# Optimization experiments

Measured on AMD Instinct MI355X. Metric: run time of the kernel, lower is better.

## Reference

```python
import jax, jax.numpy as jnp
import numpy as np

B, T, D, H = 4, 2048, 1024, 16
HD = D // H
EPS = 1e-5


def gelu_tanh(x):
    c = jnp.sqrt(jnp.asarray(2.0 / jnp.pi, x.dtype))
    return 0.5 * x * (1.0 + jnp.tanh(c * (x + 0.044715 * x * x * x)))


def layernorm(x, gamma, beta):
    mean = jnp.mean(x, axis=-1, keepdims=True)
    var = jnp.var(x, axis=-1, keepdims=True)
    return gamma * (x - mean) / jnp.sqrt(var + EPS) + beta


def setup_inputs() -> dict:
    key = jax.random.key(0)
    ks = jax.random.split(key, 12)
    s = 0.02
    return {
        "x": jax.random.normal(ks[0], (B, T, D), jnp.float32),
        "Wq": jax.random.normal(ks[1], (D, D), jnp.float32) * s,
        "Wk": jax.random.normal(ks[2], (D, D), jnp.float32) * s,
        "Wv": jax.random.normal(ks[3], (D, D), jnp.float32) * s,
        "Wo": jax.random.normal(ks[4], (D, D), jnp.float32) * s,
        "bo": jnp.zeros((D,), jnp.float32),
        "W1": jax.random.normal(ks[5], (D, 4 * D), jnp.float32) * s,
        "b1": jnp.zeros((4 * D,), jnp.float32),
        "W2": jax.random.normal(ks[6], (4 * D, D), jnp.float32) * s,
        "b2": jnp.zeros((D,), jnp.float32),
        "gamma1": jnp.ones((D,), jnp.float32),
        "beta1": jnp.zeros((D,), jnp.float32),
        "gamma2": jnp.ones((D,), jnp.float32),
        "beta2": jnp.zeros((D,), jnp.float32),
    }


def reference(x, Wq, Wk, Wv, Wo, bo, W1, b1, W2, b2, gamma1, beta1, gamma2, beta2):
    # --- attention sublayer (pre-norm, causal) ---
    h = layernorm(x, gamma1, beta1)
    q = (h @ Wq).reshape(B, T, H, HD).transpose(0, 2, 1, 3)  # (B,H,T,hd)
    k = (h @ Wk).reshape(B, T, H, HD).transpose(0, 2, 1, 3)
    v = (h @ Wv).reshape(B, T, H, HD).transpose(0, 2, 1, 3)
    scores = jnp.einsum("bhqd,bhkd->bhqk", q, k) * (HD ** -0.5)
    causal = jnp.tril(jnp.ones((T, T), bool))
    scores = jnp.where(causal, scores, -jnp.inf)
    w = jax.nn.softmax(scores, axis=-1)
    attn = jnp.einsum("bhqk,bhkd->bhqd", w, v).transpose(0, 2, 1, 3).reshape(B, T, D)
    x = x + (attn @ Wo + bo)
    # --- FFN sublayer ---
    h2 = layernorm(x, gamma2, beta2)
    ff = gelu_tanh(h2 @ W1 + b1) @ W2 + b2
    return x + ff
```

## Files before the change

### kernel.cpp

```cpp
#include <hip/hip_runtime.h>
#include <hip/hip_bf16.h>


typedef __bf16 bf16;
typedef __attribute__((ext_vector_type(8))) __bf16 bf16x8;
typedef __attribute__((ext_vector_type(4))) __bf16 bf16x4;
typedef __attribute__((ext_vector_type(4))) float floatx4;

#define EXPC 0.18033688011112042f

__device__ __forceinline__ void async_cp16(const bf16* g, bf16* l) {
  __builtin_amdgcn_global_load_lds(
      (const __attribute__((address_space(1))) void*)g,
      (__attribute__((address_space(3))) void*)l, 16, 0, 0);
}

__global__ __launch_bounds__(256) void transpose_cvt4(
    const float* __restrict__ S0, const float* __restrict__ S1,
    const float* __restrict__ S2, const float* __restrict__ S3,
    bf16* __restrict__ D0, bf16* __restrict__ D1, bf16* __restrict__ D2,
    bf16* __restrict__ D3, int K, int N) {
  const float* W = (blockIdx.z == 0) ? S0 : (blockIdx.z == 1) ? S1
                   : (blockIdx.z == 2) ? S2 : S3;
  bf16* WT = (blockIdx.z == 0) ? D0 : (blockIdx.z == 1) ? D1
             : (blockIdx.z == 2) ? D2 : D3;
  __shared__ bf16 tile[32][33];
  const int tn = blockIdx.x;
  const int tk = blockIdx.y;
  const int t = threadIdx.x;
  const int row = t >> 3;
  const int c4 = (t & 7) * 4;

  const float* src = W + (size_t)(tk * 32 + row) * N + tn * 32 + c4;
  float4 v = *(const float4*)src;
  tile[row][c4 + 0] = (bf16)v.x;
  tile[row][c4 + 1] = (bf16)v.y;
  tile[row][c4 + 2] = (bf16)v.z;
  tile[row][c4 + 3] = (bf16)v.w;
  __syncthreads();
  bf16x4 o;
  o[0] = tile[c4 + 0][row];
  o[1] = tile[c4 + 1][row];
  o[2] = tile[c4 + 2][row];
  o[3] = tile[c4 + 3][row];
  *(bf16x4*)(WT + (size_t)(tn * 32 + row) * K + tk * 32 + c4) = o;
}

__global__ __launch_bounds__(256) void transpose_cvt(
    const float* __restrict__ W, bf16* __restrict__ WT, int K, int N) {
  __shared__ bf16 tile[32][33];
  const int tn = blockIdx.x;
  const int tk = blockIdx.y;
  const int t = threadIdx.x;
  const int row = t >> 3;
  const int c4 = (t & 7) * 4;

  const float* src = W + (size_t)(tk * 32 + row) * N + tn * 32 + c4;
  float4 v = *(const float4*)src;
  tile[row][c4 + 0] = (bf16)v.x;
  tile[row][c4 + 1] = (bf16)v.y;
  tile[row][c4 + 2] = (bf16)v.z;
  tile[row][c4 + 3] = (bf16)v.w;
  __syncthreads();
  bf16x4 o;
  o[0] = tile[c4 + 0][row];
  o[1] = tile[c4 + 1][row];
  o[2] = tile[c4 + 2][row];
  o[3] = tile[c4 + 3][row];
  *(bf16x4*)(WT + (size_t)(tn * 32 + row) * K + tk * 32 + c4) = o;
}

__global__ __launch_bounds__(256) void vtrans_kernel(
    const bf16* __restrict__ QKV, bf16* __restrict__ Vt) {
  const int tt = blockIdx.x;
  const int bh = blockIdx.y;
  const int b = bh >> 4, h = bh & 15;
  __shared__ bf16 tile[64][72];
  const int t = threadIdx.x;
  const int row = t >> 3;
  const int c8 = (t & 7) * 8;
  const size_t vbase = (size_t)b * 2048 * 3072 + 2048 + (size_t)h * 64;
  const bf16* src = QKV + vbase + (size_t)(tt * 64 + row) * 3072 + c8;
  *(bf16x8*)&tile[row][c8] = *(const bf16x8*)src;
  *(bf16x8*)&tile[row + 32][c8] = *(const bf16x8*)(src + (size_t)32 * 3072);
  __syncthreads();
  bf16x8 o0, o1;
#pragma unroll
  for (int j = 0; j < 8; ++j) {
    o0[j] = tile[c8 + j][row];
    o1[j] = tile[c8 + j][row + 32];
  }
  bf16* dst = Vt + ((size_t)bh * 64 + row) * 2048 + tt * 64 + c8;
  *(bf16x8*)dst = o0;
  *(bf16x8*)(dst + (size_t)32 * 2048) = o1;
}

__global__ __launch_bounds__(256) void ln_kernel(
    const float* __restrict__ x, const float* __restrict__ gamma,
    const float* __restrict__ beta, bf16* __restrict__ out) {
  const int row = blockIdx.x;
  const int t = threadIdx.x;
  const float* xr = x + (size_t)row * 1024;
  float4 v4 = *(const float4*)(xr + t * 4);
  float a[4] = {v4.x, v4.y, v4.z, v4.w};
  float s = a[0] + a[1] + a[2] + a[3];
  float ss = a[0] * a[0] + a[1] * a[1] + a[2] * a[2] + a[3] * a[3];
  for (int off = 1; off < 64; off <<= 1) {
    s += __shfl_xor(s, off);
    ss += __shfl_xor(ss, off);
  }
  __shared__ float red[8];
  const int wid = t >> 6, lane = t & 63;
  if (lane == 0) { red[wid] = s; red[wid + 4] = ss; }
  __syncthreads();
  s = red[0] + red[1] + red[2] + red[3];
  ss = red[4] + red[5] + red[6] + red[7];
  const float mean = s * (1.0f / 1024.0f);
  const float var = ss * (1.0f / 1024.0f) - mean * mean;
  const float rstd = rsqrtf(var + 1e-5f);
  bf16x4 o;
  for (int j = 0; j < 4; ++j) {
    float g = gamma[t * 4 + j];
    float b = beta[t * 4 + j];
    o[j] = (bf16)((a[j] - mean) * rstd * g + b);
  }
  *(bf16x4*)(out + (size_t)row * 1024 + t * 4) = o;
}

__device__ __forceinline__ float gelu_f(float x) {
  const float c = 0.7978845608028654f;
  float u = c * (x + 0.044715f * x * x * x);
  u = fminf(fmaxf(u, -10.0f), 10.0f);
  float t = __builtin_exp2f(u * 2.8853900817779268f);
  return x * t * __builtin_amdgcn_rcpf(t + 1.0f);
}

template <int MODE, int BK>
__global__ __launch_bounds__(256, 2) void gemm_bt(
    const bf16* __restrict__ A, const bf16* __restrict__ BT,
    const float* __restrict__ bias, const float* __restrict__ resid,
    void* __restrict__ out, int M, int N, int K) {
  __shared__ bf16 sA[128 * BK];
  __shared__ bf16 sB[128 * BK];
  constexpr int GPR = BK / 8;
  constexpr int CPT = GPR / 2;
  constexpr int RPI = 256 / GPR;
  constexpr int SW = (BK >= 64) ? 7 : 0;

  const int t = threadIdx.x;
  const int lane = t & 63, wid = t >> 6;
  const int waveM = wid >> 1, waveN = wid & 1;
  const int quad = lane >> 4, l16 = lane & 15;
  const size_t m0 = (size_t)blockIdx.x * 128;
  const size_t n0 = (size_t)blockIdx.y * 128;

  floatx4 acc[4][4] = {};

  const int r0 = t / GPR;
  const int gp = t % GPR;
  const int gsrc = gp ^ (r0 & SW);
  const bf16* Ag = A + (m0 + r0) * (size_t)K + gsrc * 8;
  const bf16* Bg = BT + (n0 + r0) * (size_t)K + gsrc * 8;
  bf16* sAp = sA + t * 8;
  bf16* sBp = sB + t * 8;

  for (int k0 = 0; k0 < K; k0 += BK) {
    __syncthreads();
#pragma unroll
    for (int it = 0; it < CPT; ++it) {
      async_cp16(Ag + k0 + (size_t)(it * RPI) * K, sAp + it * 2048);
      async_cp16(Bg + k0 + (size_t)(it * RPI) * K, sBp + it * 2048);
    }
    __syncthreads();
#pragma unroll
    for (int ks = 0; ks < BK / 32; ++ks) {
      bf16x8 af[4], bfv[4];
#pragma unroll
      for (int i = 0; i < 4; ++i) {
        const int rowA = waveM * 64 + i * 16 + l16;
        const int g = ((ks * 4 + quad) ^ (l16 & SW)) * 8;
        af[i] = *(const bf16x8*)&sA[rowA * BK + g];
        const int rowB = waveN * 64 + i * 16 + l16;
        bfv[i] = *(const bf16x8*)&sB[rowB * BK + g];
      }
#pragma unroll
      for (int mt = 0; mt < 4; ++mt)
#pragma unroll
        for (int nt = 0; nt < 4; ++nt)
          acc[mt][nt] = __builtin_amdgcn_mfma_f32_16x16x32_bf16(
              af[mt], bfv[nt], acc[mt][nt], 0, 0, 0);
    }
  }

#pragma unroll
  for (int mt = 0; mt < 4; ++mt) {
#pragma unroll
    for (int nt = 0; nt < 4; ++nt) {
      const size_t row_base = m0 + waveM * 64 + mt * 16 + quad * 4;
      const size_t col = n0 + waveN * 64 + nt * 16 + l16;
#pragma unroll
      for (int r = 0; r < 4; ++r) {
        const size_t row = row_base + r;
        float v = acc[mt][nt][r];
        if (MODE == 1) {
          v = gelu_f(v + bias[col]);
          ((bf16*)out)[row * N + col] = (bf16)v;
        } else if (MODE == 2) {
          v += bias[col] + resid[row * N + col];
          ((float*)out)[row * N + col] = v;
        } else {
          ((bf16*)out)[row * N + col] = (bf16)v;
        }
      }
    }
  }
}

__global__ __launch_bounds__(256) void attn_kernel(
    const bf16* __restrict__ QKV, const bf16* __restrict__ Vt,
    bf16* __restrict__ O) {
  const int idx = blockIdx.x;
  const int qt = 15 - (idx >> 6);
  const int bh = idx & 63;
  const int b = bh >> 4, h = bh & 15;
  const int t = threadIdx.x;
  const int lane = t & 63, wid = t >> 6;
  const int quad = lane >> 4, l16 = lane & 15;

  __shared__ bf16 sQ[128 * 64];
  __shared__ bf16 sK[64 * 64];
  __shared__ bf16 sV[64 * 64];
  __shared__ bf16 sP[4][16][72];

  const size_t qkvbase = (size_t)b * 2048 * 3072 + (size_t)h * 64;
  const int q0 = qt * 128;

  const int r0 = t >> 3;
  const int gp = t & 7;
  const int gsw = gp ^ (r0 & 7);

  {
    const bf16* pQ = QKV + qkvbase + (size_t)(q0 + r0) * 3072 + gsw * 8;
#pragma unroll
    for (int j = 0; j < 4; ++j)
      async_cp16(pQ + (size_t)(j * 32) * 3072, sQ + j * 2048 + t * 8);
  }

  const bf16* pK = QKV + qkvbase + 1024 + (size_t)r0 * 3072 + gsw * 8;
  const bf16* pV = Vt + ((size_t)bh * 64 + r0) * 2048 + gsw * 8;
  const ptrdiff_t bumpK = (ptrdiff_t)64 * 3072;

  async_cp16(pK, sK + t * 8);
  async_cp16(pK + (size_t)32 * 3072, sK + 2048 + t * 8);
  async_cp16(pV, sV + t * 8);
  async_cp16(pV + (size_t)32 * 2048, sV + 2048 + t * 8);
  pK += bumpK;
  pV += 64;

  __syncthreads();

  bf16x8 aq[2][2];
#pragma unroll
  for (int mt = 0; mt < 2; ++mt) {
    const int row = wid * 32 + mt * 16 + l16;
#pragma unroll
    for (int ks = 0; ks < 2; ++ks)
      aq[mt][ks] =
          *(const bf16x8*)&sQ[row * 64 + (((ks * 4 + quad) ^ (row & 7)) * 8)];
  }

  float l_part[2] = {0.f, 0.f};
  floatx4 o_acc[2][4] = {};

  const int ktmax = 2 * qt + 1;
  for (int kt = 0; kt <= ktmax; ++kt) {
    if (kt) {
      asm volatile("s_waitcnt vmcnt(0)" ::: "memory");
      __builtin_amdgcn_sched_barrier(0);
      __builtin_amdgcn_s_barrier();
    }

    bf16x8 bv[4][2], bkf[4][2];
#pragma unroll
    for (int nt = 0; nt < 4; ++nt) {
      const int d = nt * 16 + l16;
#pragma unroll
      for (int ks = 0; ks < 2; ++ks)
        bv[nt][ks] =
            *(const bf16x8*)&sV[d * 64 + (((ks * 4 + quad) ^ (d & 7)) * 8)];
      const int kr = nt * 16 + l16;
      bkf[nt][0] = *(const bf16x8*)&sK[kr * 64 + ((quad ^ (kr & 7)) * 8)];
      bkf[nt][1] = *(const bf16x8*)&sK[kr * 64 + (((4 + quad) ^ (kr & 7)) * 8)];
    }
    asm volatile("s_waitcnt lgkmcnt(0)" ::: "memory");
    __builtin_amdgcn_sched_barrier(0);
    __builtin_amdgcn_s_barrier();

    if (kt < ktmax) {
      async_cp16(pK, sK + t * 8);
      async_cp16(pK + (size_t)32 * 3072, sK + 2048 + t * 8);
      async_cp16(pV, sV + t * 8);
      async_cp16(pV + (size_t)32 * 2048, sV + 2048 + t * 8);
      pK += bumpK;
      pV += 64;
    }

    float p[2][4][4];
#pragma unroll
    for (int nt = 0; nt < 4; ++nt) {
#pragma unroll
      for (int mt = 0; mt < 2; ++mt) {
        floatx4 acc = {};
        acc = __builtin_amdgcn_mfma_f32_16x16x32_bf16(bkf[nt][0], aq[mt][0],
                                                      acc, 0, 0, 0);
        acc = __builtin_amdgcn_mfma_f32_16x16x32_bf16(bkf[nt][1], aq[mt][1],
                                                      acc, 0, 0, 0);
#pragma unroll
        for (int r = 0; r < 4; ++r)
          p[mt][nt][r] = __builtin_exp2f(acc[r] * EXPC);
      }
    }

    if (kt >= ktmax - 1) {
      const int k0 = kt * 64;
#pragma unroll
      for (int mt = 0; mt < 2; ++mt) {
        const int qg = q0 + wid * 32 + mt * 16 + l16;
#pragma unroll
        for (int nt = 0; nt < 4; ++nt) {
          const int kg = k0 + nt * 16 + quad * 4;
#pragma unroll
          for (int r = 0; r < 4; ++r)
            if (kg + r > qg) p[mt][nt][r] = 0.f;
        }
      }
    }

#pragma unroll
    for (int mt = 0; mt < 2; ++mt) {
#pragma unroll
      for (int nt = 0; nt < 4; ++nt) {
        bf16x4 pk;
#pragma unroll
        for (int r = 0; r < 4; ++r) {
          l_part[mt] += p[mt][nt][r];
          pk[r] = (bf16)p[mt][nt][r];
        }
        *(bf16x4*)&sP[wid][l16][nt * 16 + quad * 4] = pk;
      }
      bf16x8 ap0 = *(const bf16x8*)&sP[wid][l16][quad * 8];
      bf16x8 ap1 = *(const bf16x8*)&sP[wid][l16][32 + quad * 8];
#pragma unroll
      for (int nt = 0; nt < 4; ++nt) {
        o_acc[mt][nt] = __builtin_amdgcn_mfma_f32_16x16x32_bf16(
            ap0, bv[nt][0], o_acc[mt][nt], 0, 0, 0);
        o_acc[mt][nt] = __builtin_amdgcn_mfma_f32_16x16x32_bf16(
            ap1, bv[nt][1], o_acc[mt][nt], 0, 0, 0);
      }
    }
  }

#pragma unroll
  for (int mt = 0; mt < 2; ++mt) {
    float lt = l_part[mt];
    lt += __shfl_xor(lt, 16);
    lt += __shfl_xor(lt, 32);
    float inv[4];
#pragma unroll
    for (int r = 0; r < 4; ++r)
      inv[r] = 1.0f / __shfl(lt, quad * 4 + r);
#pragma unroll
    for (int nt = 0; nt < 4; ++nt)
#pragma unroll
      for (int r = 0; r < 4; ++r) {
        const size_t row =
            (size_t)b * 2048 + q0 + wid * 32 + mt * 16 + quad * 4 + r;
        const size_t col = (size_t)h * 64 + nt * 16 + l16;
        O[row * 1024 + col] = (bf16)(o_acc[mt][nt][r] * inv[r]);
      }
  }
}

extern "C" void kernel_launch(void* const* d_in, const int* in_sizes, int n_in,
                              void* d_out, int out_size, void* d_ws, size_t ws_size,
                              hipStream_t stream) {
  const float* x = (const float*)d_in[0];
  const float* Wq = (const float*)d_in[1];
  const float* Wk = (const float*)d_in[2];
  const float* Wv = (const float*)d_in[3];
  const float* Wo = (const float*)d_in[4];
  const float* bo = (const float*)d_in[5];
  const float* W1 = (const float*)d_in[6];
  const float* b1 = (const float*)d_in[7];
  const float* W2 = (const float*)d_in[8];
  const float* b2 = (const float*)d_in[9];
  const float* gamma1 = (const float*)d_in[10];
  const float* beta1 = (const float*)d_in[11];
  const float* gamma2 = (const float*)d_in[12];
  const float* beta2 = (const float*)d_in[13];

  char* ws = (char*)d_ws;
  const size_t MB = (size_t)1 << 20;
  bf16* WqkvT = (bf16*)(ws + 0 * MB);
  bf16* WoT = (bf16*)(ws + 6 * MB);
  bf16* W1T = (bf16*)(ws + 8 * MB);
  bf16* W2T = (bf16*)(ws + 16 * MB);
  bf16* h1  = (bf16*)(ws + 24 * MB);
  bf16* Vt  = (bf16*)(ws + 24 * MB);
  bf16* QKVb = (bf16*)(ws + 40 * MB);
  bf16* attnb = (bf16*)(ws + 88 * MB);
  float* x1 = (float*)(ws + 104 * MB);
  bf16* h2  = (bf16*)(ws + 136 * MB);
  bf16* midb = (bf16*)(ws + 152 * MB);

  dim3 blk(256);

  transpose_cvt4<<<dim3(32, 32, 4), blk, 0, stream>>>(
      Wq, Wk, Wv, Wo, WqkvT, WqkvT + (size_t)1024 * 1024,
      WqkvT + (size_t)2048 * 1024, WoT, 1024, 1024);
  transpose_cvt<<<dim3(128, 32), blk, 0, stream>>>(W1, W1T, 1024, 4096);
  transpose_cvt<<<dim3(32, 128), blk, 0, stream>>>(W2, W2T, 4096, 1024);

  ln_kernel<<<8192, blk, 0, stream>>>(x, gamma1, beta1, h1);

  gemm_bt<3, 64><<<dim3(64, 24), blk, 0, stream>>>(h1, WqkvT, nullptr, nullptr,
                                                   QKVb, 8192, 3072, 1024);

  vtrans_kernel<<<dim3(32, 64), blk, 0, stream>>>(QKVb, Vt);

  attn_kernel<<<dim3(1024), blk, 0, stream>>>(QKVb, Vt, attnb);

  gemm_bt<2, 128><<<dim3(64, 8), blk, 0, stream>>>(attnb, WoT, bo, x, x1,
                                                   8192, 1024, 1024);

  ln_kernel<<<8192, blk, 0, stream>>>(x1, gamma2, beta2, h2);

  gemm_bt<1, 64><<<dim3(64, 32), blk, 0, stream>>>(h2, W1T, b1, nullptr, midb,
                                                   8192, 4096, 1024);

  gemm_bt<2, 128><<<dim3(64, 8), blk, 0, stream>>>(midb, W2T, b2, x1, d_out,
                                                   8192, 1024, 4096);
}
```

Before: 479.8 us.

## Merge weight transposes and first layernorm into one prep kernel; shrink BK

Combines the four weight transpose/convert launches and the first layernorm into a single kernel that dispatches on block index, removing several launches and the tail gaps between them. Separately, the Wo and W2 projection GEMMs switch from BK=128 to BK=64, which halves their shared-memory tiles and may allow more resident blocks per CU. In exchange, K-loop iterations and barriers double for those GEMMs, and the merged kernel's branch adds some per-block overhead.

```diff
diff --git a/kernel.cpp b/kernel.cpp
--- a/kernel.cpp
+++ b/kernel.cpp
@@ -15,22 +15,41 @@
       (__attribute__((address_space(3))) void*)l, 16, 0, 0);
 }
 
-__global__ __launch_bounds__(256) void transpose_cvt4(
-    const float* __restrict__ S0, const float* __restrict__ S1,
-    const float* __restrict__ S2, const float* __restrict__ S3,
-    bf16* __restrict__ D0, bf16* __restrict__ D1, bf16* __restrict__ D2,
-    bf16* __restrict__ D3, int K, int N) {
-  const float* W = (blockIdx.z == 0) ? S0 : (blockIdx.z == 1) ? S1
-                   : (blockIdx.z == 2) ? S2 : S3;
-  bf16* WT = (blockIdx.z == 0) ? D0 : (blockIdx.z == 1) ? D1
-             : (blockIdx.z == 2) ? D2 : D3;
-  __shared__ bf16 tile[32][33];
-  const int tn = blockIdx.x;
-  const int tk = blockIdx.y;
-  const int t = threadIdx.x;
+__device__ __forceinline__ void ln_body(
+    const float* __restrict__ x, const float* __restrict__ gamma,
+    const float* __restrict__ beta, bf16* __restrict__ out, int row, int t,
+    float* red) {
+  const float* xr = x + (size_t)row * 1024;
+  float4 v4 = *(const float4*)(xr + t * 4);
+  float a[4] = {v4.x, v4.y, v4.z, v4.w};
+  float s = a[0] + a[1] + a[2] + a[3];
+  float ss = a[0] * a[0] + a[1] * a[1] + a[2] * a[2] + a[3] * a[3];
+  for (int off = 1; off < 64; off <<= 1) {
+    s += __shfl_xor(s, off);
+    ss += __shfl_xor(ss, off);
+  }
+  const int wid = t >> 6, lane = t & 63;
+  if (lane == 0) { red[wid] = s; red[wid + 4] = ss; }
+  __syncthreads();
+  s = red[0] + red[1] + red[2] + red[3];
+  ss = red[4] + red[5] + red[6] + red[7];
+  const float mean = s * (1.0f / 1024.0f);
+  const float var = ss * (1.0f / 1024.0f) - mean * mean;
+  const float rstd = rsqrtf(var + 1e-5f);
+  bf16x4 o;
+  for (int j = 0; j < 4; ++j) {
+    float g = gamma[t * 4 + j];
+    float b = beta[t * 4 + j];
+    o[j] = (bf16)((a[j] - mean) * rstd * g + b);
+  }
+  *(bf16x4*)(out + (size_t)row * 1024 + t * 4) = o;
+}
+
+__device__ __forceinline__ void tc_body(
+    const float* __restrict__ W, bf16* __restrict__ WT, int K, int N, int tn,
+    int tk, int t, bf16 (*tile)[33]) {
   const int row = t >> 3;
   const int c4 = (t & 7) * 4;
-
   const float* src = W + (size_t)(tk * 32 + row) * N + tn * 32 + c4;
   float4 v = *(const float4*)src;
   tile[row][c4 + 0] = (bf16)v.x;
@@ -46,28 +65,47 @@
   *(bf16x4*)(WT + (size_t)(tn * 32 + row) * K + tk * 32 + c4) = o;
 }
 
-__global__ __launch_bounds__(256) void transpose_cvt(
-    const float* __restrict__ W, bf16* __restrict__ WT, int K, int N) {
+__global__ __launch_bounds__(256) void prep_kernel(
+    const float* __restrict__ x, const float* __restrict__ gamma1,
+    const float* __restrict__ beta1, bf16* __restrict__ h1,
+    const float* __restrict__ Wq, const float* __restrict__ Wk,
+    const float* __restrict__ Wv, const float* __restrict__ Wo,
+    bf16* __restrict__ WqT, bf16* __restrict__ WkT, bf16* __restrict__ WvT,
+    bf16* __restrict__ WoT, const float* __restrict__ W1,
+    bf16* __restrict__ W1T, const float* __restrict__ W2,
+    bf16* __restrict__ W2T) {
   __shared__ bf16 tile[32][33];
-  const int tn = blockIdx.x;
-  const int tk = blockIdx.y;
+  __shared__ float red[8];
+  const int bid = blockIdx.x;
   const int t = threadIdx.x;
-  const int row = t >> 3;
-  const int c4 = (t & 7) * 4;
-
-  const float* src = W + (size_t)(tk * 32 + row) * N + tn * 32 + c4;
-  float4 v = *(const float4*)src;
-  tile[row][c4 + 0] = (bf16)v.x;
-  tile[row][c4 + 1] = (bf16)v.y;
-  tile[row][c4 + 2] = (bf16)v.z;
-  tile[row][c4 + 3] = (bf16)v.w;
-  __syncthreads();
-  bf16x4 o;
-  o[0] = tile[c4 + 0][row];
-  o[1] = tile[c4 + 1][row];
-  o[2] = tile[c4 + 2][row];
-  o[3] = tile[c4 + 3][row];
-  *(bf16x4*)(WT + (size_t)(tn * 32 + row) * K + tk * 32 + c4) = o;
+  if (bid < 8192) {
+    ln_body(x, gamma1, beta1, h1, bid, t, red);
+  } else if (bid < 12288) {
+    const int rem = bid - 8192;
+    const int z = rem >> 10;
+    const int tk = (rem >> 5) & 31;
+    const int tn = rem & 31;
+    const float* W = (z == 0) ? Wq : (z == 1) ? Wk : (z == 2) ? Wv : Wo;
+    bf16* WT = (z == 0) ? WqT : (z == 1) ? WkT : (z == 2) ? WvT : WoT;
+    tc_body(W, WT, 1024, 1024, tn, tk, t, tile);
+  } else if (bid < 16384) {
+    const int rem = bid - 12288;
+    const int tn = rem & 127;
+    const int tk = rem >> 7;
+    tc_body(W1, W1T, 1024, 4096, tn, tk, t, tile);
+  } else {
+    const int rem = bid - 16384;
+    const int tn = rem & 31;
+    const int tk = rem >> 5;
+    tc_body(W2, W2T, 4096, 1024, tn, tk, t, tile);
+  }
+}
+
+__global__ __launch_bounds__(256) void ln_kernel(
+    const float* __restrict__ x, const float* __restrict__ gamma,
+    const float* __restrict__ beta, bf16* __restrict__ out) {
+  __shared__ float red[8];
+  ln_body(x, gamma, beta, out, blockIdx.x, threadIdx.x, red);
 }
 
 __global__ __launch_bounds__(256) void vtrans_kernel(
@@ -93,38 +131,6 @@
   bf16* dst = Vt + ((size_t)bh * 64 + row) * 2048 + tt * 64 + c8;
   *(bf16x8*)dst = o0;
   *(bf16x8*)(dst + (size_t)32 * 2048) = o1;
-}
-
-__global__ __launch_bounds__(256) void ln_kernel(
-    const float* __restrict__ x, const float* __restrict__ gamma,
-    const float* __restrict__ beta, bf16* __restrict__ out) {
-  const int row = blockIdx.x;
-  const int t = threadIdx.x;
-  const float* xr = x + (size_t)row * 1024;
-  float4 v4 = *(const float4*)(xr + t * 4);
-  float a[4] = {v4.x, v4.y, v4.z, v4.w};
-  float s = a[0] + a[1] + a[2] + a[3];
-  float ss = a[0] * a[0] + a[1] * a[1] + a[2] * a[2] + a[3] * a[3];
-  for (int off = 1; off < 64; off <<= 1) {
-    s += __shfl_xor(s, off);
-    ss += __shfl_xor(ss, off);
-  }
-  __shared__ float red[8];
-  const int wid = t >> 6, lane = t & 63;
-  if (lane == 0) { red[wid] = s; red[wid + 4] = ss; }
-  __syncthreads();
-  s = red[0] + red[1] + red[2] + red[3];
-  ss = red[4] + red[5] + red[6] + red[7];
-  const float mean = s * (1.0f / 1024.0f);
-  const float var = ss * (1.0f / 1024.0f) - mean * mean;
-  const float rstd = rsqrtf(var + 1e-5f);
-  bf16x4 o;
-  for (int j = 0; j < 4; ++j) {
-    float g = gamma[t * 4 + j];
-    float b = beta[t * 4 + j];
-    o[j] = (bf16)((a[j] - mean) * rstd * g + b);
-  }
-  *(bf16x4*)(out + (size_t)row * 1024 + t * 4) = o;
 }
 
 __device__ __forceinline__ float gelu_f(float x) {
@@ -415,13 +421,10 @@
 
   dim3 blk(256);
 
-  transpose_cvt4<<<dim3(32, 32, 4), blk, 0, stream>>>(
-      Wq, Wk, Wv, Wo, WqkvT, WqkvT + (size_t)1024 * 1024,
-      WqkvT + (size_t)2048 * 1024, WoT, 1024, 1024);
-  transpose_cvt<<<dim3(128, 32), blk, 0, stream>>>(W1, W1T, 1024, 4096);
-  transpose_cvt<<<dim3(32, 128), blk, 0, stream>>>(W2, W2T, 4096, 1024);
-
-  ln_kernel<<<8192, blk, 0, stream>>>(x, gamma1, beta1, h1);
+  prep_kernel<<<dim3(20480), blk, 0, stream>>>(
+      x, gamma1, beta1, h1, Wq, Wk, Wv, Wo, WqkvT,
+      WqkvT + (size_t)1024 * 1024, WqkvT + (size_t)2048 * 1024, WoT, W1, W1T,
+      W2, W2T);
 
   gemm_bt<3, 64><<<dim3(64, 24), blk, 0, stream>>>(h1, WqkvT, nullptr, nullptr,
                                                    QKVb, 8192, 3072, 1024);
@@ -430,14 +433,14 @@
 
   attn_kernel<<<dim3(1024), blk, 0, stream>>>(QKVb, Vt, attnb);
 
-  gemm_bt<2, 128><<<dim3(64, 8), blk, 0, stream>>>(attnb, WoT, bo, x, x1,
-                                                   8192, 1024, 1024);
+  gemm_bt<2, 64><<<dim3(64, 8), blk, 0, stream>>>(attnb, WoT, bo, x, x1,
+                                                  8192, 1024, 1024);
 
   ln_kernel<<<8192, blk, 0, stream>>>(x1, gamma2, beta2, h2);
 
   gemm_bt<1, 64><<<dim3(64, 32), blk, 0, stream>>>(h2, W1T, b1, nullptr, midb,
                                                    8192, 4096, 1024);
 
-  gemm_bt<2, 128><<<dim3(64, 8), blk, 0, stream>>>(midb, W2T, b2, x1, d_out,
-                                                   8192, 1024, 4096);
-}
+  gemm_bt<2, 64><<<dim3(64, 8), blk, 0, stream>>>(midb, W2T, b2, x1, d_out,
+                                                  8192, 1024, 4096);
+}
```

Result: slower. 490.0 us (+2.1%).
